# Performance work log

Hardware: AMD Instinct MI355X
Metric: run time of the kernel (lower is better)

The kernel has to match this reference:

```python
import jax, jax.numpy as jnp
import numpy as np

NEG = -9e15  # kept for fidelity though mask is unused in original forward

def setup_inputs() -> dict:
    key = jax.random.key(0)
    k1, k2, k3 = jax.random.split(key, 3)
    N, Fin, Fout = 8192, 512, 256
    x = jax.random.normal(k1, (N, Fin), dtype=jnp.float32)
    # xavier_uniform with gain=1.414 ~ U(-b, b), b = gain*sqrt(6/(fan_in+fan_out))
    bW = 1.414 * np.sqrt(6.0 / (Fin + Fout))
    W = jax.random.uniform(k2, (Fin, Fout), minval=-bW, maxval=bW, dtype=jnp.float32)
    ba = 1.414 * np.sqrt(6.0 / (2 * Fout + 1))
    a = jax.random.uniform(k3, (2 * Fout, 1), minval=-ba, maxval=ba, dtype=jnp.float32)
    return {"x": x, "W": W, "a": a}

def reference(x, W, a):
    # h: [N, Fout]
    h = x @ W
    Fout = h.shape[1]
    # Algebraic decomposition of additive score: e_ij = relu(a1.h_i + a2.h_j)
    a1, a2 = a[:Fout, 0], a[Fout:, 0]  # [Fout], [Fout]
    f = h @ a1  # [N] contribution of row node i
    g = h @ a2  # [N] contribution of col node j
    e = jax.nn.relu(f[:, None] + g[None, :])  # [N, N]
    attention = jax.nn.softmax(e, axis=1)
    h_prime = attention @ h  # [N, Fout]
    return jax.nn.elu(h_prime)
```

## Files before the change

### kernel.cpp

```cpp
#include <hip/hip_runtime.h>
#include <math.h>

#define NROWS 8192
#define FIN   512
#define FOUT  256
#define NCHUNK 512
#define CHROWS 16

typedef _Float16 f16;
typedef _Float16 f16x8 __attribute__((ext_vector_type(8)));
typedef float    f32x4 __attribute__((ext_vector_type(4)));

__global__ __launch_bounds__(256) void prep_wt(const float* __restrict__ W,
                                               f16* __restrict__ Wt,
                                               float* __restrict__ fg) {
    const int n = blockIdx.x, t = threadIdx.x;
    Wt[(size_t)n * FIN + t]       = (f16)W[(size_t)t * FOUT + n];
    Wt[(size_t)n * FIN + t + 256] = (f16)W[(size_t)(t + 256) * FOUT + n];
    if (n < 64) fg[n * 256 + t] = 0.f;
}

__global__ __launch_bounds__(512) void gemm_fg(const float* __restrict__ x,
                                               const f16* __restrict__ Wt,
                                               const float* __restrict__ a,
                                               f16* __restrict__ h,
                                               float* __restrict__ f,
                                               float* __restrict__ g) {
    __shared__ __align__(16) f16 As[64][136];
    __shared__ __align__(16) f16 Bs[128][136];
    __shared__ float sf[2][64], sg[2][64];
    const int tid = threadIdx.x;
    const int n0 = blockIdx.x * 128;
    const int m0 = blockIdx.y * 64;
    const int arow = tid >> 3, aseg = (tid & 7) * 16;
    const int brow = tid >> 2, bseg = (tid & 3) * 32;
    const int w = tid >> 6, lane = tid & 63;
    const int wm = (w & 3) * 16, wn = (w >> 2) * 64;
    const int l15 = lane & 15, quad = lane >> 4;

    float4 pa[4];
    f16x8 pb[4];
#pragma unroll
    for (int j = 0; j < 4; ++j) {
        pa[j] = *(const float4*)&x[(size_t)(m0 + arow) * FIN + aseg + j * 4];
        pb[j] = *(const f16x8*)&Wt[(size_t)(n0 + brow) * FIN + bseg + j * 8];
    }

    f32x4 acc[4] = {};
    for (int k0 = 0; k0 < FIN; k0 += 128) {
        __syncthreads();
        {
            f16x8 t0, t1;
            t0[0] = (f16)pa[0].x; t0[1] = (f16)pa[0].y;
            t0[2] = (f16)pa[0].z; t0[3] = (f16)pa[0].w;
            t0[4] = (f16)pa[1].x; t0[5] = (f16)pa[1].y;
            t0[6] = (f16)pa[1].z; t0[7] = (f16)pa[1].w;
            t1[0] = (f16)pa[2].x; t1[1] = (f16)pa[2].y;
            t1[2] = (f16)pa[2].z; t1[3] = (f16)pa[2].w;
            t1[4] = (f16)pa[3].x; t1[5] = (f16)pa[3].y;
            t1[6] = (f16)pa[3].z; t1[7] = (f16)pa[3].w;
            *(f16x8*)&As[arow][aseg]     = t0;
            *(f16x8*)&As[arow][aseg + 8] = t1;
        }
#pragma unroll
        for (int j = 0; j < 4; ++j)
            *(f16x8*)&Bs[brow][bseg + j * 8] = pb[j];
        __syncthreads();
        if (k0 + 128 < FIN) {
#pragma unroll
            for (int j = 0; j < 4; ++j) {
                pa[j] = *(const float4*)&x[(size_t)(m0 + arow) * FIN + k0 + 128 + aseg + j * 4];
                pb[j] = *(const f16x8*)&Wt[(size_t)(n0 + brow) * FIN + k0 + 128 + bseg + j * 8];
            }
        }
#pragma unroll
        for (int kk = 0; kk < 4; ++kk) {
            const f16x8 af = *(const f16x8*)&As[wm + l15][kk * 32 + quad * 8];
            f16x8 bf[4];
#pragma unroll
            for (int tj = 0; tj < 4; ++tj)
                bf[tj] = *(const f16x8*)&Bs[wn + tj * 16 + l15][kk * 32 + quad * 8];
#pragma unroll
            for (int tj = 0; tj < 4; ++tj)
                acc[tj] = __builtin_amdgcn_mfma_f32_16x16x32_f16(af, bf[tj], acc[tj], 0, 0, 0);
        }
    }
#pragma unroll
    for (int tj = 0; tj < 4; ++tj) {
        const int col = n0 + wn + tj * 16 + l15;
#pragma unroll
        for (int r = 0; r < 4; ++r) {
            const int row = m0 + wm + quad * 4 + r;
            h[(size_t)row * FOUT + col] = (f16)acc[tj][r];
        }
    }
    float a1c[4], a2c[4];
#pragma unroll
    for (int tj = 0; tj < 4; ++tj) {
        a1c[tj] = a[n0 + wn + tj * 16 + l15];
        a2c[tj] = a[FOUT + n0 + wn + tj * 16 + l15];
    }
    float pf[4], pg[4];
#pragma unroll
    for (int r = 0; r < 4; ++r) {
        pf[r] = acc[0][r] * a1c[0] + acc[1][r] * a1c[1]
              + acc[2][r] * a1c[2] + acc[3][r] * a1c[3];
        pg[r] = acc[0][r] * a2c[0] + acc[1][r] * a2c[1]
              + acc[2][r] * a2c[2] + acc[3][r] * a2c[3];
    }
#pragma unroll
    for (int off = 8; off >= 1; off >>= 1)
#pragma unroll
        for (int r = 0; r < 4; ++r) {
            pf[r] += __shfl_xor(pf[r], off, 16);
            pg[r] += __shfl_xor(pg[r], off, 16);
        }
    const int ng = w >> 2;
    if (l15 == 0)
#pragma unroll
        for (int r = 0; r < 4; ++r) {
            sf[ng][wm + quad * 4 + r] = pf[r];
            sg[ng][wm + quad * 4 + r] = pg[r];
        }
    __syncthreads();
    if (tid < 64) {
        atomicAdd(&f[m0 + tid], sf[0][tid] + sf[1][tid]);
        atomicAdd(&g[m0 + tid], sg[0][tid] + sg[1][tid]);
    }
}

__global__ __launch_bounds__(256) void rank_scatter(const float* __restrict__ g,
                                                    float* __restrict__ gs,
                                                    int* __restrict__ perm) {
    const int t = threadIdx.x;
    const int jl = t & 15;
    const int seg = t >> 4;
    const int j = blockIdx.x * 16 + jl;
    const float gj = g[j];
    const int base = seg * 512;
    int cnt = 0;
#pragma unroll 4
    for (int r = 0; r < 512; r += 4) {
        const float4 v = *(const float4*)&g[base + r];
        const int i0 = base + r;
        cnt += (v.x < gj) || (v.x == gj && (i0 + 0) < j);
        cnt += (v.y < gj) || (v.y == gj && (i0 + 1) < j);
        cnt += (v.z < gj) || (v.z == gj && (i0 + 2) < j);
        cnt += (v.w < gj) || (v.w == gj && (i0 + 3) < j);
    }
    __shared__ int part[16][16];
    part[seg][jl] = cnt;
    __syncthreads();
    if (seg == 0) {
        int rank = 0;
#pragma unroll
        for (int ss = 0; ss < 16; ++ss) rank += part[ss][jl];
        gs[rank] = gj;
        perm[rank] = j;
    }
}

__global__ __launch_bounds__(256) void scan_pass1(const f16* __restrict__ h,
                                                  const int* __restrict__ perm,
                                                  const float* __restrict__ gs,
                                                  const float* __restrict__ f,
                                                  float* __restrict__ c0,
                                                  float* __restrict__ c1,
                                                  float* __restrict__ c1s,
                                                  int* __restrict__ n0arr) {
    const int b = blockIdx.x, c = threadIdx.x;
    if (b < NCHUNK) {
        const int base = b * CHROWS;
        __shared__ int p[CHROWS];
        __shared__ float wl[CHROWS];
        if (c < CHROWS) {
            p[c] = perm[base + c];
            wl[c] = expf(gs[base + c] - gs[NROWS - 1]);
        }
        __syncthreads();
        float s0 = 0.f, s1 = 0.f;
        for (int r = 0; r < CHROWS; ++r) {
            float v = (float)h[(size_t)p[r] * FOUT + c];
            s0 += v;
            s1 += wl[r] * v;
        }
        c0[b * FOUT + c] = s0;
        c1[b * FOUT + c] = s1;
        if (c == 0) {
            float t = 0.f;
            for (int r = 0; r < CHROWS; ++r) t += wl[r];
            c1s[b] = t;
        }
    } else {
        const int i = (b - NCHUNK) * 256 + c;
        const float tt = -f[i];
        int lo = 0, hi = NROWS;
        while (lo < hi) {
            int mid = (lo + hi) >> 1;
            if (gs[mid] <= tt) lo = mid + 1; else hi = mid;
        }
        n0arr[i] = lo;
    }
}

__global__ __launch_bounds__(256) void scan_pass2(const float* __restrict__ c0,
                                                  const float* __restrict__ c1,
                                                  const float* __restrict__ c1s,
                                                  float* __restrict__ o0,
                                                  float* __restrict__ o1,
                                                  float* __restrict__ o1s) {
    const int b = blockIdx.x, t = threadIdx.x;
    __shared__ float sb[256];
    if (b < 256) {
        const float e0 = c0[(2 * t) * FOUT + b];
        const float e1 = c0[(2 * t + 1) * FOUT + b];
        const float local = e0 + e1;
        sb[t] = local;
        __syncthreads();
        for (int off = 1; off < 256; off <<= 1) {
            float add = (t >= off) ? sb[t - off] : 0.f;
            __syncthreads();
            sb[t] += add;
            __syncthreads();
        }
        const float ex = sb[t] - local;
        o0[(2 * t) * FOUT + b] = ex;
        o0[(2 * t + 1) * FOUT + b] = ex + e0;
    } else if (b < 512) {
        const int col = b - 256;
        const float e0 = c1[(2 * t) * FOUT + col];
        const float e1 = c1[(2 * t + 1) * FOUT + col];
        const float local = e0 + e1;
        sb[t] = local;
        __syncthreads();
        for (int off = 1; off < 256; off <<= 1) {
            float add = (t + off < 256) ? sb[t + off] : 0.f;
            __syncthreads();
            sb[t] += add;
            __syncthreads();
        }
        const float exs = sb[t] - local;
        o1[(2 * t) * FOUT + col] = exs + e1;
        o1[(2 * t + 1) * FOUT + col] = exs;
    } else {
        const float e0 = c1s[2 * t];
        const float e1 = c1s[2 * t + 1];
        const float local = e0 + e1;
        sb[t] = local;
        __syncthreads();
        for (int off = 1; off < 256; off <<= 1) {
            float add = (t + off < 256) ? sb[t + off] : 0.f;
            __syncthreads();
            sb[t] += add;
            __syncthreads();
        }
        const float exs = sb[t] - local;
        o1s[2 * t] = exs + e1;
        o1s[2 * t + 1] = exs;
    }
}

__global__ __launch_bounds__(256) void scan_pass3(const f16* __restrict__ h,
                                                  const int* __restrict__ perm,
                                                  const float* __restrict__ gs,
                                                  const float* __restrict__ o0,
                                                  const float* __restrict__ o1,
                                                  const float* __restrict__ o1s,
                                                  f16* __restrict__ P0,
                                                  f16* __restrict__ S1,
                                                  float* __restrict__ S1s) {
    const int k = blockIdx.x, c = threadIdx.x;
    const int base = k * CHROWS;
    __shared__ int p[CHROWS];
    __shared__ float wl[CHROWS];
    if (c < CHROWS) {
        p[c] = perm[base + c];
        wl[c] = expf(gs[base + c] - gs[NROWS - 1]);
    }
    __syncthreads();
    float run0 = o0[k * FOUT + c];
    for (int r = 0; r < CHROWS; ++r) {
        P0[(size_t)(base + r) * FOUT + c] = (f16)run0;
        run0 += (float)h[(size_t)p[r] * FOUT + c];
    }
    float run1 = o1[k * FOUT + c];
    for (int r = CHROWS - 1; r >= 0; --r) {
        run1 += wl[r] * (float)h[(size_t)p[r] * FOUT + c];
        S1[(size_t)(base + r) * FOUT + c] = (f16)run1;
    }
    if (c == 0) {
        float rs = o1s[k];
        for (int r = CHROWS - 1; r >= 0; --r) { rs += wl[r]; S1s[base + r] = rs; }
    }
    if (k == NCHUNK - 1) {
        P0[(size_t)NROWS * FOUT + c] = (f16)run0;
        S1[(size_t)NROWS * FOUT + c] = (f16)0.f;
        if (c == 0) S1s[NROWS] = 0.f;
    }
}

__global__ __launch_bounds__(256) void final_kernel(const float* __restrict__ f,
                                                    const float* __restrict__ gs,
                                                    const int* __restrict__ n0arr,
                                                    const f16* __restrict__ P0,
                                                    const f16* __restrict__ S1,
                                                    const float* __restrict__ S1s,
                                                    float* __restrict__ out) {
    const int b = blockIdx.x, c = threadIdx.x;
    const float gm = gs[NROWS - 1];
#pragma unroll
    for (int rr = 0; rr < 4; ++rr) {
        const int i = b * 4 + rr;
        const float fi = f[i];
        const int n0 = n0arr[i];
        const float m = fmaxf(0.f, fi + gm);
        const float A = expf(-m);
        const float B = expf(fi + gm - m);
        const float denom = A * (float)n0 + B * S1s[n0];
        const float numer = A * (float)P0[(size_t)n0 * FOUT + c]
                          + B * (float)S1[(size_t)n0 * FOUT + c];
        const float v = numer / denom;
        out[(size_t)i * FOUT + c] = v > 0.f ? v : expm1f(v);
    }
}

extern "C" void kernel_launch(void* const* d_in, const int* in_sizes, int n_in,
                              void* d_out, int out_size, void* d_ws, size_t ws_size,
                              hipStream_t stream) {
    (void)in_sizes; (void)n_in; (void)out_size; (void)ws_size;
    const float* x = (const float*)d_in[0];
    const float* W = (const float*)d_in[1];
    const float* a = (const float*)d_in[2];
    float* out = (float*)d_out;

    char* ws = (char*)d_ws;
    size_t off = 0;
    auto alloc = [&](size_t bytes) -> void* {
        void* p = ws + off;
        off += (bytes + 255) & ~(size_t)255;
        return p;
    };
    f16*   Wt   = (f16*)alloc((size_t)FOUT * FIN * 2);
    f16*   h    = (f16*)alloc((size_t)NROWS * FOUT * 2);
    f16*   P0   = (f16*)alloc((size_t)(NROWS + 1) * FOUT * 2);
    f16*   S1   = (f16*)alloc((size_t)(NROWS + 1) * FOUT * 2);
    float* fg   = (float*)alloc(2 * NROWS * 4);
    float* f    = fg;
    float* g    = fg + NROWS;
    float* gs   = (float*)alloc(NROWS * 4);
    int*   perm = (int*)alloc(NROWS * 4);
    int*   n0arr= (int*)alloc(NROWS * 4);
    float* c0   = (float*)alloc(NCHUNK * FOUT * 4);
    float* c1   = (float*)alloc(NCHUNK * FOUT * 4);
    float* o0   = (float*)alloc(NCHUNK * FOUT * 4);
    float* o1   = (float*)alloc(NCHUNK * FOUT * 4);
    float* c1s  = (float*)alloc(NCHUNK * 4);
    float* o1s  = (float*)alloc(NCHUNK * 4);
    float* S1s  = (float*)alloc((NROWS + 1) * 4);

    prep_wt<<<256, 256, 0, stream>>>(W, Wt, fg);
    gemm_fg<<<dim3(FOUT / 128, NROWS / 64), 512, 0, stream>>>(x, Wt, a, h, f, g);
    rank_scatter<<<NROWS / 16, 256, 0, stream>>>(g, gs, perm);
    scan_pass1<<<NCHUNK + 32, 256, 0, stream>>>(h, perm, gs, f, c0, c1, c1s, n0arr);
    scan_pass2<<<513, 256, 0, stream>>>(c0, c1, c1s, o0, o1, o1s);
    scan_pass3<<<NCHUNK, 256, 0, stream>>>(h, perm, gs, o0, o1, o1s, P0, S1, S1s);
    final_kernel<<<NROWS / 4, 256, 0, stream>>>(f, gs, n0arr, P0, S1, S1s, out);
}
```

Baseline: 117.6 us.

## Fuse scan pass3 into final kernel by recomputing in-chunk prefix sums

Result: slower. 133.5 us (+13.5%).

```diff
diff --git a/kernel.cpp b/kernel.cpp
--- a/kernel.cpp
+++ b/kernel.cpp
@@ -260,65 +260,53 @@
     }
 }
 
-__global__ __launch_bounds__(256) void scan_pass3(const f16* __restrict__ h,
-                                                  const int* __restrict__ perm,
-                                                  const float* __restrict__ gs,
-                                                  const float* __restrict__ o0,
-                                                  const float* __restrict__ o1,
-                                                  const float* __restrict__ o1s,
-                                                  f16* __restrict__ P0,
-                                                  f16* __restrict__ S1,
-                                                  float* __restrict__ S1s) {
-    const int k = blockIdx.x, c = threadIdx.x;
-    const int base = k * CHROWS;
-    __shared__ int p[CHROWS];
-    __shared__ float wl[CHROWS];
-    if (c < CHROWS) {
-        p[c] = perm[base + c];
-        wl[c] = expf(gs[base + c] - gs[NROWS - 1]);
-    }
-    __syncthreads();
-    float run0 = o0[k * FOUT + c];
-    for (int r = 0; r < CHROWS; ++r) {
-        P0[(size_t)(base + r) * FOUT + c] = (f16)run0;
-        run0 += (float)h[(size_t)p[r] * FOUT + c];
-    }
-    float run1 = o1[k * FOUT + c];
-    for (int r = CHROWS - 1; r >= 0; --r) {
-        run1 += wl[r] * (float)h[(size_t)p[r] * FOUT + c];
-        S1[(size_t)(base + r) * FOUT + c] = (f16)run1;
-    }
-    if (c == 0) {
-        float rs = o1s[k];
-        for (int r = CHROWS - 1; r >= 0; --r) { rs += wl[r]; S1s[base + r] = rs; }
-    }
-    if (k == NCHUNK - 1) {
-        P0[(size_t)NROWS * FOUT + c] = (f16)run0;
-        S1[(size_t)NROWS * FOUT + c] = (f16)0.f;
-        if (c == 0) S1s[NROWS] = 0.f;
-    }
-}
-
 __global__ __launch_bounds__(256) void final_kernel(const float* __restrict__ f,
                                                     const float* __restrict__ gs,
                                                     const int* __restrict__ n0arr,
-                                                    const f16* __restrict__ P0,
-                                                    const f16* __restrict__ S1,
-                                                    const float* __restrict__ S1s,
+                                                    const int* __restrict__ perm,
+                                                    const f16* __restrict__ h,
+                                                    const float* __restrict__ o0,
+                                                    const float* __restrict__ o1,
+                                                    const float* __restrict__ o1s,
                                                     float* __restrict__ out) {
     const int b = blockIdx.x, c = threadIdx.x;
     const float gm = gs[NROWS - 1];
+    __shared__ int pS[4][CHROWS];
+    __shared__ float wlS[4][CHROWS];
+    __shared__ int kS[4];
+    if (c < 4) {
+        const int n0 = n0arr[b * 4 + c];
+        kS[c] = min(n0 >> 4, NCHUNK - 1);
+    }
+    __syncthreads();
+    if (c < 64) {
+        const int rr = c >> 4, r = c & 15;
+        const int base = kS[rr] << 4;
+        pS[rr][r] = perm[base + r];
+        wlS[rr][r] = expf(gs[base + r] - gm);
+    }
+    __syncthreads();
 #pragma unroll
     for (int rr = 0; rr < 4; ++rr) {
         const int i = b * 4 + rr;
         const float fi = f[i];
         const int n0 = n0arr[i];
+        const int k = kS[rr];
+        const int r0 = n0 - (k << 4);
+        float p0 = o0[k * FOUT + c];
+        for (int r = 0; r < r0; ++r)
+            p0 += (float)h[(size_t)pS[rr][r] * FOUT + c];
+        float s1 = o1[k * FOUT + c];
+        float s1s = o1s[k];
+        for (int r = CHROWS - 1; r >= r0; --r) {
+            s1 += wlS[rr][r] * (float)h[(size_t)pS[rr][r] * FOUT + c];
+            s1s += wlS[rr][r];
+        }
         const float m = fmaxf(0.f, fi + gm);
         const float A = expf(-m);
         const float B = expf(fi + gm - m);
-        const float denom = A * (float)n0 + B * S1s[n0];
-        const float numer = A * (float)P0[(size_t)n0 * FOUT + c]
-                          + B * (float)S1[(size_t)n0 * FOUT + c];
+        const float denom = A * (float)n0 + B * s1s;
+        const float numer = A * p0 + B * s1;
         const float v = numer / denom;
         out[(size_t)i * FOUT + c] = v > 0.f ? v : expm1f(v);
     }
@@ -342,8 +330,6 @@
     };
     f16*   Wt   = (f16*)alloc((size_t)FOUT * FIN * 2);
     f16*   h    = (f16*)alloc((size_t)NROWS * FOUT * 2);
-    f16*   P0   = (f16*)alloc((size_t)(NROWS + 1) * FOUT * 2);
-    f16*   S1   = (f16*)alloc((size_t)(NROWS + 1) * FOUT * 2);
     float* fg   = (float*)alloc(2 * NROWS * 4);
     float* f    = fg;
     float* g    = fg + NROWS;
@@ -356,13 +342,11 @@
     float* o1   = (float*)alloc(NCHUNK * FOUT * 4);
     float* c1s  = (float*)alloc(NCHUNK * 4);
     float* o1s  = (float*)alloc(NCHUNK * 4);
-    float* S1s  = (float*)alloc((NROWS + 1) * 4);
 
     prep_wt<<<256, 256, 0, stream>>>(W, Wt, fg);
     gemm_fg<<<dim3(FOUT / 128, NROWS / 64), 512, 0, stream>>>(x, Wt, a, h, f, g);
     rank_scatter<<<NROWS / 16, 256, 0, stream>>>(g, gs, perm);
     scan_pass1<<<NCHUNK + 32, 256, 0, stream>>>(h, perm, gs, f, c0, c1, c1s, n0arr);
     scan_pass2<<<513, 256, 0, stream>>>(c0, c1, c1s, o0, o1, o1s);
-    scan_pass3<<<NCHUNK, 256, 0, stream>>>(h, perm, gs, o0, o1, o1s, P0, S1, S1s);
-    final_kernel<<<NROWS / 4, 256, 0, stream>>>(f, gs, n0arr, P0, S1, S1s, out);
-}
+    final_kernel<<<NROWS / 4, 256, 0, stream>>>(f, gs, n0arr, perm, h, o0, o1, o1s, out);
+}
```

## Drop weight-prep kernel; load fp32 W directly in GEMM and write partial f/g

Applied to the files above, without the earlier changes.

New measurement: 121.6 us. 1.03x slower.

```diff
diff --git a/kernel.cpp b/kernel.cpp
--- a/kernel.cpp
+++ b/kernel.cpp
@@ -11,21 +11,12 @@
 typedef _Float16 f16x8 __attribute__((ext_vector_type(8)));
 typedef float    f32x4 __attribute__((ext_vector_type(4)));
 
-__global__ __launch_bounds__(256) void prep_wt(const float* __restrict__ W,
-                                               f16* __restrict__ Wt,
-                                               float* __restrict__ fg) {
-    const int n = blockIdx.x, t = threadIdx.x;
-    Wt[(size_t)n * FIN + t]       = (f16)W[(size_t)t * FOUT + n];
-    Wt[(size_t)n * FIN + t + 256] = (f16)W[(size_t)(t + 256) * FOUT + n];
-    if (n < 64) fg[n * 256 + t] = 0.f;
-}
-
 __global__ __launch_bounds__(512) void gemm_fg(const float* __restrict__ x,
-                                               const f16* __restrict__ Wt,
+                                               const float* __restrict__ W,
                                                const float* __restrict__ a,
                                                f16* __restrict__ h,
-                                               float* __restrict__ f,
-                                               float* __restrict__ g) {
+                                               float* __restrict__ fpart,
+                                               float* __restrict__ gpart) {
     __shared__ __align__(16) f16 As[64][136];
     __shared__ __align__(16) f16 Bs[128][136];
     __shared__ float sf[2][64], sg[2][64];
@@ -33,18 +24,21 @@
     const int n0 = blockIdx.x * 128;
     const int m0 = blockIdx.y * 64;
     const int arow = tid >> 3, aseg = (tid & 7) * 16;
-    const int brow = tid >> 2, bseg = (tid & 3) * 32;
+    const int bn = tid & 127, bks = (tid >> 7) * 32;
     const int w = tid >> 6, lane = tid & 63;
     const int wm = (w & 3) * 16, wn = (w >> 2) * 64;
     const int l15 = lane & 15, quad = lane >> 4;
 
     float4 pa[4];
-    f16x8 pb[4];
-#pragma unroll
-    for (int j = 0; j < 4; ++j) {
+    float  pw[32];
+#pragma unroll
+    for (int j = 0; j < 4; ++j)
         pa[j] = *(const float4*)&x[(size_t)(m0 + arow) * FIN + aseg + j * 4];
-        pb[j] = *(const f16x8*)&Wt[(size_t)(n0 + brow) * FIN + bseg + j * 8];
-    }
+#pragma unroll
+    for (int j = 0; j < 4; ++j)
+#pragma unroll
+        for (int e = 0; e < 8; ++e)
+            pw[j * 8 + e] = W[(size_t)(bks + j * 8 + e) * FOUT + n0 + bn];
 
     f32x4 acc[4] = {};
     for (int k0 = 0; k0 < FIN; k0 += 128) {
@@ -63,15 +57,23 @@
             *(f16x8*)&As[arow][aseg + 8] = t1;
         }
 #pragma unroll
-        for (int j = 0; j < 4; ++j)
-            *(f16x8*)&Bs[brow][bseg + j * 8] = pb[j];
+        for (int j = 0; j < 4; ++j) {
+            f16x8 tb;
+#pragma unroll
+            for (int e = 0; e < 8; ++e)
+                tb[e] = (f16)pw[j * 8 + e];
+            *(f16x8*)&Bs[bn][bks + j * 8] = tb;
+        }
         __syncthreads();
         if (k0 + 128 < FIN) {
 #pragma unroll
-            for (int j = 0; j < 4; ++j) {
+            for (int j = 0; j < 4; ++j)
                 pa[j] = *(const float4*)&x[(size_t)(m0 + arow) * FIN + k0 + 128 + aseg + j * 4];
-                pb[j] = *(const f16x8*)&Wt[(size_t)(n0 + brow) * FIN + k0 + 128 + bseg + j * 8];
-            }
+#pragma unroll
+            for (int j = 0; j < 4; ++j)
+#pragma unroll
+                for (int e = 0; e < 8; ++e)
+                    pw[j * 8 + e] = W[(size_t)(k0 + 128 + bks + j * 8 + e) * FOUT + n0 + bn];
         }
 #pragma unroll
         for (int kk = 0; kk < 4; ++kk) {
@@ -124,29 +126,32 @@
         }
     __syncthreads();
     if (tid < 64) {
-        atomicAdd(&f[m0 + tid], sf[0][tid] + sf[1][tid]);
-        atomicAdd(&g[m0 + tid], sg[0][tid] + sg[1][tid]);
-    }
-}
-
-__global__ __launch_bounds__(256) void rank_scatter(const float* __restrict__ g,
+        fpart[(size_t)blockIdx.x * NROWS + m0 + tid] = sf[0][tid] + sf[1][tid];
+        gpart[(size_t)blockIdx.x * NROWS + m0 + tid] = sg[0][tid] + sg[1][tid];
+    }
+}
+
+__global__ __launch_bounds__(256) void rank_scatter(const float* __restrict__ gpart,
                                                     float* __restrict__ gs,
                                                     int* __restrict__ perm) {
     const int t = threadIdx.x;
     const int jl = t & 15;
     const int seg = t >> 4;
     const int j = blockIdx.x * 16 + jl;
-    const float gj = g[j];
+    const float gj = gpart[j] + gpart[NROWS + j];
     const int base = seg * 512;
     int cnt = 0;
 #pragma unroll 4
     for (int r = 0; r < 512; r += 4) {
-        const float4 v = *(const float4*)&g[base + r];
+        const float4 v0 = *(const float4*)&gpart[base + r];
+        const float4 v1 = *(const float4*)&gpart[NROWS + base + r];
         const int i0 = base + r;
-        cnt += (v.x < gj) || (v.x == gj && (i0 + 0) < j);
-        cnt += (v.y < gj) || (v.y == gj && (i0 + 1) < j);
-        cnt += (v.z < gj) || (v.z == gj && (i0 + 2) < j);
-        cnt += (v.w < gj) || (v.w == gj && (i0 + 3) < j);
+        const float g0 = v0.x + v1.x, g1 = v0.y + v1.y;
+        const float g2 = v0.z + v1.z, g3 = v0.w + v1.w;
+        cnt += (g0 < gj) || (g0 == gj && (i0 + 0) < j);
+        cnt += (g1 < gj) || (g1 == gj && (i0 + 1) < j);
+        cnt += (g2 < gj) || (g2 == gj && (i0 + 2) < j);
+        cnt += (g3 < gj) || (g3 == gj && (i0 + 3) < j);
     }
     __shared__ int part[16][16];
     part[seg][jl] = cnt;
@@ -163,7 +168,7 @@
 __global__ __launch_bounds__(256) void scan_pass1(const f16* __restrict__ h,
                                                   const int* __restrict__ perm,
                                                   const float* __restrict__ gs,
-                                                  const float* __restrict__ f,
+                                                  const float* __restrict__ fpart,
                                                   float* __restrict__ c0,
                                                   float* __restrict__ c1,
                                                   float* __restrict__ c1s,
@@ -193,7 +198,7 @@
         }
     } else {
         const int i = (b - NCHUNK) * 256 + c;
-        const float tt = -f[i];
+        const float tt = -(fpart[i] + fpart[NROWS + i]);
         int lo = 0, hi = NROWS;
         while (lo < hi) {
             int mid = (lo + hi) >> 1;
@@ -299,7 +304,7 @@
     }
 }
 
-__global__ __launch_bounds__(256) void final_kernel(const float* __restrict__ f,
+__global__ __launch_bounds__(256) void final_kernel(const float* __restrict__ fpart,
                                                     const float* __restrict__ gs,
                                                     const int* __restrict__ n0arr,
                                                     const f16* __restrict__ P0,
@@ -311,7 +316,7 @@
 #pragma unroll
     for (int rr = 0; rr < 4; ++rr) {
         const int i = b * 4 + rr;
-        const float fi = f[i];
+        const float fi = fpart[i] + fpart[NROWS + i];
         const int n0 = n0arr[i];
         const float m = fmaxf(0.f, fi + gm);
         const float A = expf(-m);
@@ -340,29 +345,26 @@
         off += (bytes + 255) & ~(size_t)255;
         return p;
     };
-    f16*   Wt   = (f16*)alloc((size_t)FOUT * FIN * 2);
-    f16*   h    = (f16*)alloc((size_t)NROWS * FOUT * 2);
-    f16*   P0   = (f16*)alloc((size_t)(NROWS + 1) * FOUT * 2);
-    f16*   S1   = (f16*)alloc((size_t)(NROWS + 1) * FOUT * 2);
-    float* fg   = (float*)alloc(2 * NROWS * 4);
-    float* f    = fg;
-    float* g    = fg + NROWS;
-    float* gs   = (float*)alloc(NROWS * 4);
-    int*   perm = (int*)alloc(NROWS * 4);
-    int*   n0arr= (int*)alloc(NROWS * 4);
-    float* c0   = (float*)alloc(NCHUNK * FOUT * 4);
-    float* c1   = (float*)alloc(NCHUNK * FOUT * 4);
-    float* o0   = (float*)alloc(NCHUNK * FOUT * 4);
-    float* o1   = (float*)alloc(NCHUNK * FOUT * 4);
-    float* c1s  = (float*)alloc(NCHUNK * 4);
-    float* o1s  = (float*)alloc(NCHUNK * 4);
-    float* S1s  = (float*)alloc((NROWS + 1) * 4);
-
-    prep_wt<<<256, 256, 0, stream>>>(W, Wt, fg);
-    gemm_fg<<<dim3(FOUT / 128, NROWS / 64), 512, 0, stream>>>(x, Wt, a, h, f, g);
-    rank_scatter<<<NROWS / 16, 256, 0, stream>>>(g, gs, perm);
-    scan_pass1<<<NCHUNK + 32, 256, 0, stream>>>(h, perm, gs, f, c0, c1, c1s, n0arr);
+    f16*   h     = (f16*)alloc((size_t)NROWS * FOUT * 2);
+    f16*   P0    = (f16*)alloc((size_t)(NROWS + 1) * FOUT * 2);
+    f16*   S1    = (f16*)alloc((size_t)(NROWS + 1) * FOUT * 2);
+    float* fpart = (float*)alloc(2 * NROWS * 4);
+    float* gpart = (float*)alloc(2 * NROWS * 4);
+    float* gs    = (float*)alloc(NROWS * 4);
+    int*   perm  = (int*)alloc(NROWS * 4);
+    int*   n0arr = (int*)alloc(NROWS * 4);
+    float* c0    = (float*)alloc(NCHUNK * FOUT * 4);
+    float* c1    = (float*)alloc(NCHUNK * FOUT * 4);
+    float* o0    = (float*)alloc(NCHUNK * FOUT * 4);
+    float* o1    = (float*)alloc(NCHUNK * FOUT * 4);
+    float* c1s   = (float*)alloc(NCHUNK * 4);
+    float* o1s   = (float*)alloc(NCHUNK * 4);
+    float* S1s   = (float*)alloc((NROWS + 1) * 4);
+
+    gemm_fg<<<dim3(FOUT / 128, NROWS / 64), 512, 0, stream>>>(x, W, a, h, fpart, gpart);
+    rank_scatter<<<NROWS / 16, 256, 0, stream>>>(gpart, gs, perm);
+    scan_pass1<<<NCHUNK + 32, 256, 0, stream>>>(h, perm, gs, fpart, c0, c1, c1s, n0arr);
     scan_pass2<<<513, 256, 0, stream>>>(c0, c1, c1s, o0, o1, o1s);
     scan_pass3<<<NCHUNK, 256, 0, stream>>>(h, perm, gs, o0, o1, o1s, P0, S1, S1s);
-    final_kernel<<<NROWS / 4, 256, 0, stream>>>(f, gs, n0arr, P0, S1, S1s, out);
-}
+    final_kernel<<<NROWS / 4, 256, 0, stream>>>(fpart, gs, n0arr, P0, S1, S1s, out);
+}
```

## Fuse final output into scan pass3 by bucketing query rows per chunk

Applied to the files above, without the earlier changes.

Measured after the change: 122.5 us. 1.04x slower.

```diff
diff --git a/kernel.cpp b/kernel.cpp
--- a/kernel.cpp
+++ b/kernel.cpp
@@ -13,11 +13,16 @@
 
 __global__ __launch_bounds__(256) void prep_wt(const float* __restrict__ W,
                                                f16* __restrict__ Wt,
-                                               float* __restrict__ fg) {
+                                               float* __restrict__ fg,
+                                               int* __restrict__ bcount) {
     const int n = blockIdx.x, t = threadIdx.x;
     Wt[(size_t)n * FIN + t]       = (f16)W[(size_t)t * FOUT + n];
     Wt[(size_t)n * FIN + t + 256] = (f16)W[(size_t)(t + 256) * FOUT + n];
     if (n < 64) fg[n * 256 + t] = 0.f;
+    if (n < 3) {
+        const int idx = n * 256 + t;
+        if (idx < 513) bcount[idx] = 0;
+    }
 }
 
 __global__ __launch_bounds__(512) void gemm_fg(const float* __restrict__ x,
@@ -167,7 +172,8 @@
                                                   float* __restrict__ c0,
                                                   float* __restrict__ c1,
                                                   float* __restrict__ c1s,
-                                                  int* __restrict__ n0arr) {
+                                                  int* __restrict__ bcount,
+                                                  int* __restrict__ bitems) {
     const int b = blockIdx.x, c = threadIdx.x;
     if (b < NCHUNK) {
         const int base = b * CHROWS;
@@ -199,7 +205,10 @@
             int mid = (lo + hi) >> 1;
             if (gs[mid] <= tt) lo = mid + 1; else hi = mid;
         }
-        n0arr[i] = lo;
+        const int bkt = lo >> 4;
+        const int r0 = lo & 15;
+        const int pos = atomicAdd(&bcount[bkt], 1);
+        bitems[(size_t)bkt * NROWS + pos] = i | (r0 << 16);
     }
 }
 
@@ -266,13 +275,17 @@
                                                   const float* __restrict__ o0,
                                                   const float* __restrict__ o1,
                                                   const float* __restrict__ o1s,
-                                                  f16* __restrict__ P0,
-                                                  f16* __restrict__ S1,
-                                                  float* __restrict__ S1s) {
+                                                  const float* __restrict__ f,
+                                                  const int* __restrict__ bcount,
+                                                  const int* __restrict__ bitems,
+                                                  float* __restrict__ out) {
     const int k = blockIdx.x, c = threadIdx.x;
     const int base = k * CHROWS;
     __shared__ int p[CHROWS];
     __shared__ float wl[CHROWS];
+    __shared__ float p0L[CHROWS][FOUT];
+    __shared__ float s1L[CHROWS][FOUT];
+    __shared__ float s1sL[CHROWS];
     if (c < CHROWS) {
         p[c] = perm[base + c];
         wl[c] = expf(gs[base + c] - gs[NROWS - 1]);
@@ -280,47 +293,49 @@
     __syncthreads();
     float run0 = o0[k * FOUT + c];
     for (int r = 0; r < CHROWS; ++r) {
-        P0[(size_t)(base + r) * FOUT + c] = (f16)run0;
+        p0L[r][c] = run0;
         run0 += (float)h[(size_t)p[r] * FOUT + c];
     }
     float run1 = o1[k * FOUT + c];
     for (int r = CHROWS - 1; r >= 0; --r) {
         run1 += wl[r] * (float)h[(size_t)p[r] * FOUT + c];
-        S1[(size_t)(base + r) * FOUT + c] = (f16)run1;
+        s1L[r][c] = run1;
     }
     if (c == 0) {
         float rs = o1s[k];
-        for (int r = CHROWS - 1; r >= 0; --r) { rs += wl[r]; S1s[base + r] = rs; }
-    }
-    if (k == NCHUNK - 1) {
-        P0[(size_t)NROWS * FOUT + c] = (f16)run0;
-        S1[(size_t)NROWS * FOUT + c] = (f16)0.f;
-        if (c == 0) S1s[NROWS] = 0.f;
-    }
-}
-
-__global__ __launch_bounds__(256) void final_kernel(const float* __restrict__ f,
-                                                    const float* __restrict__ gs,
-                                                    const int* __restrict__ n0arr,
-                                                    const f16* __restrict__ P0,
-                                                    const f16* __restrict__ S1,
-                                                    const float* __restrict__ S1s,
-                                                    float* __restrict__ out) {
-    const int b = blockIdx.x, c = threadIdx.x;
+        for (int r = CHROWS - 1; r >= 0; --r) { rs += wl[r]; s1sL[r] = rs; }
+    }
+    __syncthreads();
     const float gm = gs[NROWS - 1];
-#pragma unroll
-    for (int rr = 0; rr < 4; ++rr) {
-        const int i = b * 4 + rr;
+    const int cnt = bcount[k];
+    for (int t = 0; t < cnt; ++t) {
+        const int packed = bitems[(size_t)k * NROWS + t];
+        const int i = packed & 0xFFFF;
+        const int r0 = packed >> 16;
         const float fi = f[i];
-        const int n0 = n0arr[i];
         const float m = fmaxf(0.f, fi + gm);
         const float A = expf(-m);
         const float B = expf(fi + gm - m);
-        const float denom = A * (float)n0 + B * S1s[n0];
-        const float numer = A * (float)P0[(size_t)n0 * FOUT + c]
-                          + B * (float)S1[(size_t)n0 * FOUT + c];
+        const float denom = A * (float)(base + r0) + B * s1sL[r0];
+        const float numer = A * p0L[r0][c] + B * s1L[r0][c];
         const float v = numer / denom;
         out[(size_t)i * FOUT + c] = v > 0.f ? v : expm1f(v);
+    }
+    if (k == NCHUNK - 1) {
+        const int cnt2 = bcount[NCHUNK];
+        for (int t = 0; t < cnt2; ++t) {
+            const int packed = bitems[(size_t)NCHUNK * NROWS + t];
+            const int i = packed & 0xFFFF;
+            const float fi = f[i];
+            const float m = fmaxf(0.f, fi + gm);
+            const float A = expf(-m);
+            const float B = expf(fi + gm - m);
+            (void)B;
+            const float denom = A * (float)NROWS;
+            const float numer = A * run0;
+            const float v = numer / denom;
+            out[(size_t)i * FOUT + c] = v > 0.f ? v : expm1f(v);
+        }
     }
 }
 
@@ -340,29 +355,26 @@
         off += (bytes + 255) & ~(size_t)255;
         return p;
     };
-    f16*   Wt   = (f16*)alloc((size_t)FOUT * FIN * 2);
-    f16*   h    = (f16*)alloc((size_t)NROWS * FOUT * 2);
-    f16*   P0   = (f16*)alloc((size_t)(NROWS + 1) * FOUT * 2);
-    f16*   S1   = (f16*)alloc((size_t)(NROWS + 1) * FOUT * 2);
-    float* fg   = (float*)alloc(2 * NROWS * 4);
-    float* f    = fg;
-    float* g    = fg + NROWS;
-    float* gs   = (float*)alloc(NROWS * 4);
-    int*   perm = (int*)alloc(NROWS * 4);
-    int*   n0arr= (int*)alloc(NROWS * 4);
-    float* c0   = (float*)alloc(NCHUNK * FOUT * 4);
-    float* c1   = (float*)alloc(NCHUNK * FOUT * 4);
-    float* o0   = (float*)alloc(NCHUNK * FOUT * 4);
-    float* o1   = (float*)alloc(NCHUNK * FOUT * 4);
-    float* c1s  = (float*)alloc(NCHUNK * 4);
-    float* o1s  = (float*)alloc(NCHUNK * 4);
-    float* S1s  = (float*)alloc((NROWS + 1) * 4);
-
-    prep_wt<<<256, 256, 0, stream>>>(W, Wt, fg);
+    f16*   Wt    = (f16*)alloc((size_t)FOUT * FIN * 2);
+    f16*   h     = (f16*)alloc((size_t)NROWS * FOUT * 2);
+    float* fg    = (float*)alloc(2 * NROWS * 4);
+    float* f     = fg;
+    float* g     = fg + NROWS;
+    float* gs    = (float*)alloc(NROWS * 4);
+    int*   perm  = (int*)alloc(NROWS * 4);
+    float* c0    = (float*)alloc(NCHUNK * FOUT * 4);
+    float* c1    = (float*)alloc(NCHUNK * FOUT * 4);
+    float* o0    = (float*)alloc(NCHUNK * FOUT * 4);
+    float* o1    = (float*)alloc(NCHUNK * FOUT * 4);
+    float* c1s   = (float*)alloc(NCHUNK * 4);
+    float* o1s   = (float*)alloc(NCHUNK * 4);
+    int*   bcount= (int*)alloc((NCHUNK + 1) * 4);
+    int*   bitems= (int*)alloc((size_t)(NCHUNK + 1) * NROWS * 4);
+
+    prep_wt<<<256, 256, 0, stream>>>(W, Wt, fg, bcount);
     gemm_fg<<<dim3(FOUT / 128, NROWS / 64), 512, 0, stream>>>(x, Wt, a, h, f, g);
     rank_scatter<<<NROWS / 16, 256, 0, stream>>>(g, gs, perm);
-    scan_pass1<<<NCHUNK + 32, 256, 0, stream>>>(h, perm, gs, f, c0, c1, c1s, n0arr);
+    scan_pass1<<<NCHUNK + 32, 256, 0, stream>>>(h, perm, gs, f, c0, c1, c1s, bcount, bitems);
     scan_pass2<<<513, 256, 0, stream>>>(c0, c1, c1s, o0, o1, o1s);
-    scan_pass3<<<NCHUNK, 256, 0, stream>>>(h, perm, gs, o0, o1, o1s, P0, S1, S1s);
-    final_kernel<<<NROWS / 4, 256, 0, stream>>>(f, gs, n0arr, P0, S1, S1s, out);
-}
+    scan_pass3<<<NCHUNK, 256, 0, stream>>>(h, perm, gs, o0, o1, o1s, f, bcount, bitems, out);
+}
```
